# Kernel optimization log

Hardware: AMD Instinct MI355X
Metric: run time of the kernel (lower is better)

The kernel has to match this reference:

```python
import jax, jax.numpy as jnp
import numpy as np

B, T, E = 4, 2048, 1024
H = 16
HS = E // H  # head_size = d_model // num_heads, d_model == E here
D_FF = 4 * E
EPS = 1e-5


def _layernorm(x, g, b):
    mu = jnp.mean(x, axis=-1, keepdims=True)
    var = jnp.var(x, axis=-1, keepdims=True)
    return (x - mu) * jax.lax.rsqrt(var + EPS) * g + b


def setup_inputs() -> dict:
    key = jax.random.key(0)
    ks = jax.random.split(key, 12)
    s_e = 1.0 / np.sqrt(E)
    s_ff = 1.0 / np.sqrt(D_FF)
    return {
        "x": jax.random.normal(ks[0], (B, T, E), jnp.float32),
        "ln1_g": jnp.ones((E,), jnp.float32),
        "ln1_b": jnp.zeros((E,), jnp.float32),
        "Wq": jax.random.normal(ks[1], (E, E), jnp.float32) * s_e,
        "bq": jnp.zeros((E,), jnp.float32),
        "Wk": jax.random.normal(ks[2], (E, E), jnp.float32) * s_e,
        "bk": jnp.zeros((E,), jnp.float32),
        "Wv": jax.random.normal(ks[3], (E, E), jnp.float32) * s_e,
        "bv": jnp.zeros((E,), jnp.float32),
        "Wp": jax.random.normal(ks[4], (E, E), jnp.float32) * s_e,
        "bp": jnp.zeros((E,), jnp.float32),
        "ln2_g": jnp.ones((E,), jnp.float32),
        "ln2_b": jnp.zeros((E,), jnp.float32),
        "W1": jax.random.normal(ks[5], (E, D_FF), jnp.float32) * s_e,
        "b1": jnp.zeros((D_FF,), jnp.float32),
        "W2": jax.random.normal(ks[6], (D_FF, E), jnp.float32) * s_ff,
        "b2": jnp.zeros((E,), jnp.float32),
    }


def reference(x, ln1_g, ln1_b, Wq, bq, Wk, bk, Wv, bv, Wp, bp,
              ln2_g, ln2_b, W1, b1, W2, b2):
    # --- attention sublayer ---
    h = _layernorm(x, ln1_g, ln1_b)                      # [B,T,E]
    q = (h @ Wq + bq).reshape(B, T, H, HS)
    k = (h @ Wk + bk).reshape(B, T, H, HS)
    v = (h @ Wv + bv).reshape(B, T, H, HS)
    scores = jnp.einsum('bqhd,bkhd->bhqk', q, k) * (HS ** -0.5)  # [B,H,T,T]
    causal = jnp.tril(jnp.ones((T, T), bool))
    scores = jnp.where(causal, scores, -jnp.inf)
    w = jax.nn.softmax(scores, axis=-1)
    attn = jnp.einsum('bhqk,bkhd->bqhd', w, v).reshape(B, T, H * HS)
    x = x + attn @ Wp + bp
    # --- FFN sublayer ---
    h2 = _layernorm(x, ln2_g, ln2_b)
    x = x + jax.nn.relu(h2 @ W1 + b1) @ W2 + b2
    return x
```

## Files before the change

### kernel.cpp

```cpp
#include <hip/hip_runtime.h>
#include <hip/hip_bf16.h>

#define B_ 4
#define T_ 2048
#define E_ 1024
#define H_ 16
#define HS_ 64
#define DFF_ 4096
#define M_ (B_ * T_)
#define LDQ_ (3 * E_)

typedef __bf16 bf16_t;
typedef __bf16 bf16x4 __attribute__((ext_vector_type(4)));
typedef __bf16 bf16x8 __attribute__((ext_vector_type(8)));
typedef float f32x4 __attribute__((ext_vector_type(4)));

#define AS1 __attribute__((address_space(1)))
#define AS3 __attribute__((address_space(3)))

__device__ __forceinline__ void gload_lds16(const void* g, void* l) {
  __builtin_amdgcn_global_load_lds((AS1 void*)(g), (AS3 void*)(l), 16, 0, 0);
}

__global__ __launch_bounds__(256) void wtrans_kernel(
    const float* __restrict__ W, bf16_t* __restrict__ Wt, int Krows, int Ncols) {
  __shared__ float tile[32][33];
  int tx = threadIdx.x, ty = threadIdx.y;
  int n0 = blockIdx.x * 32, k0 = blockIdx.y * 32;
#pragma unroll
  for (int i = 0; i < 32; i += 8)
    tile[ty + i][tx] = W[(long)(k0 + ty + i) * Ncols + n0 + tx];
  __syncthreads();
#pragma unroll
  for (int i = 0; i < 32; i += 8)
    Wt[(long)(n0 + ty + i) * Krows + k0 + tx] = (bf16_t)tile[tx][ty + i];
}

__global__ __launch_bounds__(256) void bcat_kernel(const float* a, const float* b,
                                                   const float* c, float* o) {
  int i = blockIdx.x * 256 + threadIdx.x;
  o[i] = i < 1024 ? a[i] : (i < 2048 ? b[i - 1024] : c[i - 2048]);
}

__global__ __launch_bounds__(256) void layernorm_kernel(
    const float* __restrict__ in, const float* __restrict__ g,
    const float* __restrict__ b, bf16_t* __restrict__ out) {
  int row = blockIdx.x;
  int tid = threadIdx.x;
  const float4* inr = (const float4*)(in + (long)row * E_);
  float4 v = inr[tid];
  float s = v.x + v.y + v.z + v.w;
  float ss = v.x * v.x + v.y * v.y + v.z * v.z + v.w * v.w;
#pragma unroll
  for (int o = 32; o; o >>= 1) {
    s += __shfl_xor(s, o);
    ss += __shfl_xor(ss, o);
  }
  __shared__ float red[8];
  int wv = tid >> 6;
  if ((tid & 63) == 0) {
    red[wv] = s;
    red[4 + wv] = ss;
  }
  __syncthreads();
  s = red[0] + red[1] + red[2] + red[3];
  ss = red[4] + red[5] + red[6] + red[7];
  float mu = s * (1.f / E_);
  float var = ss * (1.f / E_) - mu * mu;
  float rs = rsqrtf(var + 1e-5f);
  int ci = tid * 4;
  float4 gv = *(const float4*)(g + ci);
  float4 bv = *(const float4*)(b + ci);
  long o0 = (long)row * E_ + ci;
  out[o0 + 0] = (bf16_t)((v.x - mu) * rs * gv.x + bv.x);
  out[o0 + 1] = (bf16_t)((v.y - mu) * rs * gv.y + bv.y);
  out[o0 + 2] = (bf16_t)((v.z - mu) * rs * gv.z + bv.z);
  out[o0 + 3] = (bf16_t)((v.w - mu) * rs * gv.w + bv.w);
}

template <int RELU>
__global__ __launch_bounds__(512, 2) void gemm256_kernel(
    const bf16_t* __restrict__ A, const bf16_t* __restrict__ Bt,
    const float* __restrict__ bias, bf16_t* __restrict__ out, int N, int K) {
  __shared__ bf16_t As0[256 * 32], As1[256 * 32], As2[256 * 32], As3[256 * 32];
  __shared__ bf16_t Bs0[256 * 32], Bs1[256 * 32], Bs2[256 * 32], Bs3[256 * 32];
  const int tid = threadIdx.x;
  const int wave = tid >> 6;
  const int lane = tid & 63;
  const int wr = wave >> 2;
  const int wc = wave & 3;
  const int quad = lane >> 4, l16 = lane & 15;

  const int gx = gridDim.x;
  const int id = blockIdx.y * gx + blockIdx.x;
  const int xcd = id & 7;
  const int k_ = id >> 3;
  const int bxr = k_ % gx;
  const int byr = (k_ / gx) * 8 + xcd;
  const long rowBase = (long)byr * 256;
  const long colBase = (long)bxr * 256;

  f32x4 acc[8][4] = {};

  const int ntiles = K >> 5;

  auto stageA = [&](bf16_t* dst, int t) {
    const int k0 = t << 5;
#pragma unroll
    for (int p = 0; p < 2; ++p) {
      int idx = p * 512 + tid;
      int row = idx >> 2;
      int col = (idx & 3) * 8;
      gload_lds16(&A[(rowBase + row) * K + k0 + col],
                  dst + (p * 512 + wave * 64) * 8);
    }
  };
  auto stageB = [&](bf16_t* dst, int t) {
    const int k0 = t << 5;
#pragma unroll
    for (int p = 0; p < 2; ++p) {
      int idx = p * 512 + tid;
      int row = idx >> 2;
      int col = (idx & 3) * 8;
      gload_lds16(&Bt[(colBase + row) * K + k0 + col],
                  dst + (p * 512 + wave * 64) * 8);
    }
  };

  auto tileStep = [&](int t, const bf16_t* as, const bf16_t* bs, bf16_t* nA,
                      bf16_t* nB) {
    const bool pre = (t + 3 < ntiles);
    bf16x8 bfrag[4];
#pragma unroll
    for (int fc = 0; fc < 4; ++fc)
      bfrag[fc] = *(const bf16x8*)&bs[(wc * 64 + fc * 16 + l16) * 32 + quad * 8];

    {
      bf16x8 afrag[4];
#pragma unroll
      for (int fr = 0; fr < 4; ++fr)
        afrag[fr] =
            *(const bf16x8*)&as[(wr * 128 + fr * 16 + l16) * 32 + quad * 8];
      if (pre) stageA(nA, t + 3);
      __builtin_amdgcn_s_setprio(1);
#pragma unroll
      for (int fr = 0; fr < 4; ++fr)
#pragma unroll
        for (int fc = 0; fc < 4; ++fc)
          acc[fr][fc] = __builtin_amdgcn_mfma_f32_16x16x32_bf16(
              afrag[fr], bfrag[fc], acc[fr][fc], 0, 0, 0);
      __builtin_amdgcn_s_setprio(0);
      __builtin_amdgcn_s_barrier();
    }
    {
      bf16x8 afrag[4];
#pragma unroll
      for (int fr = 0; fr < 4; ++fr)
        afrag[fr] = *(const bf16x8*)&as[(wr * 128 + 64 + fr * 16 + l16) * 32 +
                                        quad * 8];
      if (pre) stageB(nB, t + 3);
      __builtin_amdgcn_s_setprio(1);
#pragma unroll
      for (int fr = 0; fr < 4; ++fr)
#pragma unroll
        for (int fc = 0; fc < 4; ++fc)
          acc[4 + fr][fc] = __builtin_amdgcn_mfma_f32_16x16x32_bf16(
              afrag[fr], bfrag[fc], acc[4 + fr][fc], 0, 0, 0);
      __builtin_amdgcn_s_setprio(0);
      if (t + 3 < ntiles)
        asm volatile("s_waitcnt vmcnt(8)" ::: "memory");
      else if (t + 2 < ntiles)
        asm volatile("s_waitcnt vmcnt(4)" ::: "memory");
      else if (t + 1 < ntiles)
        asm volatile("s_waitcnt vmcnt(0)" ::: "memory");
      if (t + 1 < ntiles) __builtin_amdgcn_s_barrier();
    }
  };

  stageA(As0, 0); stageB(Bs0, 0);
  stageA(As1, 1); stageB(Bs1, 1);
  stageA(As2, 2); stageB(Bs2, 2);
  asm volatile("s_waitcnt vmcnt(8)" ::: "memory");
  __builtin_amdgcn_s_barrier();

  for (int t = 0; t < ntiles; t += 4) {
    tileStep(t + 0, As0, Bs0, As3, Bs3);
    tileStep(t + 1, As1, Bs1, As0, Bs0);
    tileStep(t + 2, As2, Bs2, As1, Bs1);
    tileStep(t + 3, As3, Bs3, As2, Bs2);
  }

#pragma unroll
  for (int mh = 0; mh < 2; ++mh)
#pragma unroll
    for (int fr = 0; fr < 4; ++fr)
#pragma unroll
      for (int fc = 0; fc < 4; ++fc) {
        int colg = (int)colBase + wc * 64 + fc * 16 + l16;
        float bv = bias[colg];
#pragma unroll
        for (int r = 0; r < 4; ++r) {
          long rowg = rowBase + wr * 128 + mh * 64 + fr * 16 + quad * 4 + r;
          float v = acc[mh * 4 + fr][fc][r] + bv;
          if (RELU) v = fmaxf(v, 0.f);
          out[rowg * N + colg] = (bf16_t)v;
        }
      }
}

template <int MODE>
__global__ __launch_bounds__(512, 1) void gemm256x128_kernel(
    const bf16_t* __restrict__ A, const bf16_t* __restrict__ Bt,
    const float* __restrict__ bias, const float* __restrict__ resid,
    void* __restrict__ out, bf16_t* __restrict__ vt_out, int N, int K) {
  __shared__ bf16_t As0[256 * 32], As1[256 * 32], As2[256 * 32], As3[256 * 32];
  __shared__ bf16_t Bs0[128 * 32], Bs1[128 * 32], Bs2[128 * 32], Bs3[128 * 32];
  const int tid = threadIdx.x;
  const int wave = tid >> 6;
  const int lane = tid & 63;
  const int wr = wave >> 1;
  const int wc = wave & 1;
  const int quad = lane >> 4, l16 = lane & 15;

  const int gx = gridDim.x;
  const int id = blockIdx.y * gx + blockIdx.x;
  const int xcd = id & 7;
  const int k_ = id >> 3;
  const int bxr = k_ % gx;
  const int byr = (k_ / gx) * 8 + xcd;
  const long rowBase = (long)byr * 256;
  const long colBase = (long)bxr * 128;

  f32x4 acc[4][4] = {};

  const int ntiles = K >> 5;

  auto stageA = [&](bf16_t* dst, int t) {
    const int k0 = t << 5;
#pragma unroll
    for (int p = 0; p < 2; ++p) {
      int idx = p * 512 + tid;
      int row = idx >> 2;
      int col = (idx & 3) * 8;
      gload_lds16(&A[(rowBase + row) * K + k0 + col],
                  dst + (p * 512 + wave * 64) * 8);
    }
  };
  auto stageB = [&](bf16_t* dst, int t) {
    const int k0 = t << 5;
    int row = tid >> 2;
    int col = (tid & 3) * 8;
    gload_lds16(&Bt[(colBase + row) * K + k0 + col], dst + (wave * 64) * 8);
  };

  auto tileStep = [&](int t, const bf16_t* as, const bf16_t* bs, bf16_t* nA,
                      bf16_t* nB) {
    const bool pre = (t + 3 < ntiles);
    bf16x8 bfrag[4];
#pragma unroll
    for (int fc = 0; fc < 4; ++fc)
      bfrag[fc] = *(const bf16x8*)&bs[(wc * 64 + fc * 16 + l16) * 32 + quad * 8];

    {
      bf16x8 afrag[2];
#pragma unroll
      for (int fr = 0; fr < 2; ++fr)
        afrag[fr] =
            *(const bf16x8*)&as[(wr * 64 + fr * 16 + l16) * 32 + quad * 8];
      if (pre) stageA(nA, t + 3);
      __builtin_amdgcn_s_setprio(1);
#pragma unroll
      for (int fr = 0; fr < 2; ++fr)
#pragma unroll
        for (int fc = 0; fc < 4; ++fc)
          acc[fr][fc] = __builtin_amdgcn_mfma_f32_16x16x32_bf16(
              afrag[fr], bfrag[fc], acc[fr][fc], 0, 0, 0);
      __builtin_amdgcn_s_setprio(0);
      __builtin_amdgcn_s_barrier();
    }
    {
      bf16x8 afrag[2];
#pragma unroll
      for (int fr = 2; fr < 4; ++fr)
        afrag[fr - 2] =
            *(const bf16x8*)&as[(wr * 64 + fr * 16 + l16) * 32 + quad * 8];
      if (pre) stageB(nB, t + 3);
      __builtin_amdgcn_s_setprio(1);
#pragma unroll
      for (int fr = 2; fr < 4; ++fr)
#pragma unroll
        for (int fc = 0; fc < 4; ++fc)
          acc[fr][fc] = __builtin_amdgcn_mfma_f32_16x16x32_bf16(
              afrag[fr - 2], bfrag[fc], acc[fr][fc], 0, 0, 0);
      __builtin_amdgcn_s_setprio(0);
      if (t + 3 < ntiles)
        asm volatile("s_waitcnt vmcnt(6)" ::: "memory");
      else if (t + 2 < ntiles)
        asm volatile("s_waitcnt vmcnt(3)" ::: "memory");
      else if (t + 1 < ntiles)
        asm volatile("s_waitcnt vmcnt(0)" ::: "memory");
      if (t + 1 < ntiles) __builtin_amdgcn_s_barrier();
    }
  };

  stageA(As0, 0); stageB(Bs0, 0);
  stageA(As1, 1); stageB(Bs1, 1);
  stageA(As2, 2); stageB(Bs2, 2);
  asm volatile("s_waitcnt vmcnt(6)" ::: "memory");
  __builtin_amdgcn_s_barrier();

  for (int t = 0; t < ntiles; t += 4) {
    tileStep(t + 0, As0, Bs0, As3, Bs3);
    tileStep(t + 1, As1, Bs1, As0, Bs0);
    tileStep(t + 2, As2, Bs2, As1, Bs1);
    tileStep(t + 3, As3, Bs3, As2, Bs2);
  }

#pragma unroll
  for (int fr = 0; fr < 4; ++fr)
#pragma unroll
    for (int fc = 0; fc < 4; ++fc) {
      int colg = (int)colBase + wc * 64 + fc * 16 + l16;
      float bv = bias[colg];
#pragma unroll
      for (int r = 0; r < 4; ++r) {
        long rowg = rowBase + wr * 64 + fr * 16 + quad * 4 + r;
        float v = acc[fr][fc][r] + bv;
        long idx = rowg * N + colg;
        if (MODE == 1) {
          ((float*)out)[idx] = v + resid[idx];
        } else {
          ((bf16_t*)out)[idx] = (bf16_t)v;
          if (MODE == 2 && colg >= 2 * E_) {
            int d = colg & 63;
            int hh2 = (colg - 2 * E_) >> 6;
            int bb = (int)(rowg >> 11);
            int tt = (int)(rowg & 2047);
            vt_out[(((long)(bb * 16 + hh2)) * 64 + d) * T_ + tt] = (bf16_t)v;
          }
        }
      }
    }
}

__global__ __launch_bounds__(512) void flash_attn_kernel(
    const bf16_t* __restrict__ qkv, const bf16_t* __restrict__ vt,
    bf16_t* __restrict__ attn, bf16_t* __restrict__ Opart,
    float* __restrict__ mlpart) {
  int gx = 14 - (int)blockIdx.x;
  int pt = 0, sp = 0;
  for (int p = 0; p < 8; ++p) {
    int ns = (2 * p + 1) / 6 + 1;
    if (gx < ns) { pt = p; sp = gx; break; }
    gx -= ns;
  }

  const int tid = threadIdx.x;
  const int wave = tid >> 6;
  const int half = wave >> 2;
  const int wsub = wave & 3;
  const int lane = tid & 63;
  const int quad = lane >> 4, l16 = lane & 15;
  const int bh = blockIdx.y, b = bh >> 4, hh = bh & 15;

  const int ti = 2 * pt + half;
  const int nsplit = ti / 6 + 1;
  const int qw = ti * 128 + wsub * 32;
  const int jbeg = 12 * sp;
  const int jendU = min(12 * sp + 12, 4 * pt + 4);

  __shared__ __align__(16) bf16_t Ks[2][64 * 64];
  __shared__ __align__(16) bf16_t Vs[2][64 * 64];
  __shared__ __align__(16) bf16_t Ps[8][16 * 64];

  const bf16_t* qb = qkv;
  const bf16_t* kb = qkv + E_;

  bf16x8 aq[2][2];
#pragma unroll
  for (int s = 0; s < 2; ++s) {
    long base = (long)(b * T_ + qw + s * 16 + l16) * LDQ_ + hh * HS_ + quad * 8;
    aq[s][0] = *(const bf16x8*)&qb[base];
    aq[s][1] = *(const bf16x8*)&qb[base + 32];
#pragma unroll
    for (int e = 0; e < 8; ++e) {
      aq[s][0][e] = (bf16_t)((float)aq[s][0][e] * 0.125f);
      aq[s][1][e] = (bf16_t)((float)aq[s][1][e] * 0.125f);
    }
  }

  f32x4 o[2][4] = {};
  float lsum[2] = {};

  auto stage = [&](int buf, int j) {
    const int kv0 = j * 64;
    int row = tid >> 3;
    int gcol = ((tid & 7) ^ (row & 7)) * 8;
    gload_lds16(&kb[(long)(b * T_ + kv0 + row) * LDQ_ + hh * HS_ + gcol],
                &Ks[buf][wave * 512]);
    gload_lds16(&vt[((long)bh * HS_ + row) * T_ + kv0 + gcol],
                &Vs[buf][wave * 512]);
  };

  stage(0, jbeg);
  __syncthreads();

  for (int j = jbeg; j < jendU; ++j) {
    const int kv0 = j * 64;
    const int cur = (j - jbeg) & 1;
    if (j + 1 < jendU) stage(cur ^ 1, j + 1);
    const bf16_t* KsL = Ks[cur];
    const bf16_t* VsL = Vs[cur];
    bf16_t* Pw = Ps[wave];

#pragma unroll
    for (int s = 0; s < 2; ++s) {
      const int qs = qw + s * 16;
      if (kv0 <= qs + 15) {
        f32x4 sc[4];
        __builtin_amdgcn_s_setprio(1);
#pragma unroll
        for (int sub = 0; sub < 4; ++sub) {
          const int rk = sub * 16 + l16;
          const int k0 = rk * 64 + ((quad ^ (rk & 7)) * 8);
          f32x4 t = {};
          t = __builtin_amdgcn_mfma_f32_16x16x32_bf16(
              *(const bf16x8*)&KsL[k0], aq[s][0], t, 0, 0, 0);
          t = __builtin_amdgcn_mfma_f32_16x16x32_bf16(
              *(const bf16x8*)&KsL[k0 ^ 32], aq[s][1], t, 0, 0, 0);
          sc[sub] = t;
        }
        __builtin_amdgcn_s_setprio(0);
        if (kv0 + 63 > qs) {
          int qcol = qs + l16;
#pragma unroll
          for (int sub = 0; sub < 4; ++sub)
#pragma unroll
            for (int r = 0; r < 4; ++r) {
              int kvrow = kv0 + sub * 16 + quad * 4 + r;
              if (kvrow > qcol) sc[sub][r] = -INFINITY;
            }
        }
        float part = 0.f;
#pragma unroll
        for (int sub = 0; sub < 4; ++sub) {
#pragma unroll
          for (int r = 0; r < 4; ++r) sc[sub][r] = __expf(sc[sub][r]);
          part += (sc[sub][0] + sc[sub][1]) + (sc[sub][2] + sc[sub][3]);
        }
        lsum[s] += part;
#pragma unroll
        for (int sub = 0; sub < 4; ++sub) {
          bf16x4 pk;
#pragma unroll
          for (int r = 0; r < 4; ++r) pk[r] = (bf16_t)sc[sub][r];
          const int ch = sub * 2 + (quad >> 1);
          const int off = ((ch ^ (l16 & 7)) * 8) + ((quad & 1) * 4);
          *(bf16x4*)&Pw[l16 * 64 + off] = pk;
        }
        const int p0 = l16 * 64 + ((quad ^ (l16 & 7)) * 8);
        bf16x8 ap0 = *(const bf16x8*)&Pw[p0];
        bf16x8 ap1 = *(const bf16x8*)&Pw[p0 ^ 32];
        __builtin_amdgcn_s_setprio(1);
#pragma unroll
        for (int nt = 0; nt < 4; ++nt) {
          const int rv = nt * 16 + l16;
          const int v0 = rv * 64 + ((quad ^ (rv & 7)) * 8);
          o[s][nt] = __builtin_amdgcn_mfma_f32_16x16x32_bf16(
              *(const bf16x8*)&VsL[v0], ap0, o[s][nt], 0, 0, 0);
          o[s][nt] = __builtin_amdgcn_mfma_f32_16x16x32_bf16(
              *(const bf16x8*)&VsL[v0 ^ 32], ap1, o[s][nt], 0, 0, 0);
        }
        __builtin_amdgcn_s_setprio(0);
      }
    }
    __syncthreads();
  }

  float lval[2];
#pragma unroll
  for (int s = 0; s < 2; ++s) {
    float v = lsum[s];
    v += __shfl_xor(v, 16);
    v += __shfl_xor(v, 32);
    lval[s] = v;
  }

  if (nsplit == 1) {
#pragma unroll
    for (int s = 0; s < 2; ++s) {
      float inv = 1.f / lval[s];
      long rowg = (long)b * T_ + qw + s * 16 + l16;
#pragma unroll
      for (int nt = 0; nt < 4; ++nt) {
        bf16x4 pk;
#pragma unroll
        for (int r = 0; r < 4; ++r) pk[r] = (bf16_t)(o[s][nt][r] * inv);
        *(bf16x4*)&attn[rowg * E_ + hh * HS_ + nt * 16 + quad * 4] = pk;
      }
    }
  } else {
    int idx = (ti < 12) ? (ti - 6) * 2 + sp : 12 + (ti - 12) * 3 + sp;
    long slot = (long)bh * 24 + idx;
    bf16_t* op = Opart + slot * (128 * 64);
    float* ml = mlpart + slot * 256;
#pragma unroll
    for (int s = 0; s < 2; ++s) {
      float inv = 1.f / lval[s];
      int rloc = wsub * 32 + s * 16 + l16;
#pragma unroll
      for (int nt = 0; nt < 4; ++nt) {
        bf16x4 pk;
#pragma unroll
        for (int r = 0; r < 4; ++r) pk[r] = (bf16_t)(o[s][nt][r] * inv);
        *(bf16x4*)&op[rloc * 64 + nt * 16 + quad * 4] = pk;
      }
      if (quad == 0) ml[rloc] = lval[s];
    }
  }
}

__global__ __launch_bounds__(256) void flash_merge_kernel(
    const bf16_t* __restrict__ Opart, const float* __restrict__ mlpart,
    bf16_t* __restrict__ attn) {
  int ti = 6 + blockIdx.x;
  int bh = blockIdx.y, b = bh >> 4, hh = bh & 15;
  int ns = ti / 6 + 1;
  int base_idx = (ti < 12) ? (ti - 6) * 2 : 12 + (ti - 12) * 3;
  int r = threadIdx.x >> 1;
  int dh = (threadIdx.x & 1) * 32;

  float w[3], den = 0.f;
  for (int s = 0; s < ns; ++s) {
    long slot = (long)bh * 24 + base_idx + s;
    w[s] = mlpart[slot * 256 + r];
    den += w[s];
  }
  float inv = 1.f / den;
  float acc[32];
#pragma unroll
  for (int d = 0; d < 32; ++d) acc[d] = 0.f;
  for (int s = 0; s < ns; ++s) {
    long slot = (long)bh * 24 + base_idx + s;
    const bf16_t* op = Opart + slot * (128 * 64) + r * 64 + dh;
#pragma unroll
    for (int d = 0; d < 32; ++d) acc[d] += w[s] * (float)op[d];
  }
  long rowg = (long)b * T_ + ti * 128 + r;
  bf16_t* dst = attn + rowg * E_ + hh * HS_ + dh;
#pragma unroll
  for (int d = 0; d < 32; ++d) dst[d] = (bf16_t)(acc[d] * inv);
}

extern "C" void kernel_launch(void* const* d_in, const int* in_sizes, int n_in,
                              void* d_out, int out_size, void* d_ws,
                              size_t ws_size, hipStream_t stream) {
  const float* x = (const float*)d_in[0];
  const float* ln1_g = (const float*)d_in[1];
  const float* ln1_b = (const float*)d_in[2];
  const float* Wq = (const float*)d_in[3];
  const float* bq = (const float*)d_in[4];
  const float* Wk = (const float*)d_in[5];
  const float* bk = (const float*)d_in[6];
  const float* Wv = (const float*)d_in[7];
  const float* bv = (const float*)d_in[8];
  const float* Wp = (const float*)d_in[9];
  const float* bp = (const float*)d_in[10];
  const float* ln2_g = (const float*)d_in[11];
  const float* ln2_b = (const float*)d_in[12];
  const float* W1 = (const float*)d_in[13];
  const float* b1 = (const float*)d_in[14];
  const float* W2 = (const float*)d_in[15];
  const float* b2 = (const float*)d_in[16];
  float* out = (float*)d_out;

  const size_t MB = 1ull << 20;
  char* ws = (char*)d_ws;
  bf16_t* wqkvt = (bf16_t*)(ws + 0 * MB);
  bf16_t* wpt   = (bf16_t*)(ws + 6 * MB);
  bf16_t* w1t   = (bf16_t*)(ws + 8 * MB);
  bf16_t* w2t   = (bf16_t*)(ws + 16 * MB);
  float*  bqkv  = (float*)(ws + 24 * MB);
  bf16_t* h     = (bf16_t*)(ws + 25 * MB);
  bf16_t* qkvb  = (bf16_t*)(ws + 41 * MB);
  bf16_t* vt    = (bf16_t*)(ws + 89 * MB);
  float*  xmid  = (float*)(ws + 105 * MB);
  bf16_t* Opart = (bf16_t*)(ws + 105 * MB);
  float* mlpart = (float*)(ws + 131 * MB);
  bf16_t* attn  = h;
  bf16_t* h2    = h;
  bf16_t* ff1   = qkvb;

  dim3 tb(32, 8);
  wtrans_kernel<<<dim3(E_ / 32, E_ / 32), tb, 0, stream>>>(Wq, wqkvt, E_, E_);
  wtrans_kernel<<<dim3(E_ / 32, E_ / 32), tb, 0, stream>>>(Wk, wqkvt + (long)E_ * E_, E_, E_);
  wtrans_kernel<<<dim3(E_ / 32, E_ / 32), tb, 0, stream>>>(Wv, wqkvt + 2l * E_ * E_, E_, E_);
  wtrans_kernel<<<dim3(E_ / 32, E_ / 32), tb, 0, stream>>>(Wp, wpt, E_, E_);
  wtrans_kernel<<<dim3(DFF_ / 32, E_ / 32), tb, 0, stream>>>(W1, w1t, E_, DFF_);
  wtrans_kernel<<<dim3(E_ / 32, DFF_ / 32), tb, 0, stream>>>(W2, w2t, DFF_, E_);
  bcat_kernel<<<12, 256, 0, stream>>>(bq, bk, bv, bqkv);

  layernorm_kernel<<<M_, 256, 0, stream>>>(x, ln1_g, ln1_b, h);

  gemm256x128_kernel<2><<<dim3(3 * E_ / 128, M_ / 256), 512, 0, stream>>>(
      h, wqkvt, bqkv, nullptr, qkvb, vt, 3 * E_, E_);

  flash_attn_kernel<<<dim3(15, B_ * H_), 512, 0, stream>>>(qkvb, vt, attn,
                                                           Opart, mlpart);
  flash_merge_kernel<<<dim3(10, B_ * H_), 256, 0, stream>>>(Opart, mlpart, attn);

  gemm256x128_kernel<1><<<dim3(E_ / 128, M_ / 256), 512, 0, stream>>>(
      attn, wpt, bp, x, xmid, nullptr, E_, E_);

  layernorm_kernel<<<M_, 256, 0, stream>>>(xmid, ln2_g, ln2_b, h2);

  gemm256_kernel<1><<<dim3(DFF_ / 256, M_ / 256), 512, 0, stream>>>(
      h2, w1t, b1, ff1, DFF_, E_);
  gemm256x128_kernel<1><<<dim3(E_ / 128, M_ / 256), 512, 0, stream>>>(
      ff1, w2t, b2, xmid, out, nullptr, E_, DFF_);
}
```

Baseline: 512.3 us.

## Cut GEMM LDS to triple buffering for two blocks per CU; split V transpose

```diff
diff --git a/kernel.cpp b/kernel.cpp
--- a/kernel.cpp
+++ b/kernel.cpp
@@ -209,12 +209,12 @@
 }
 
 template <int MODE>
-__global__ __launch_bounds__(512, 1) void gemm256x128_kernel(
+__global__ __launch_bounds__(512, 2) void gemm256x128_kernel(
     const bf16_t* __restrict__ A, const bf16_t* __restrict__ Bt,
     const float* __restrict__ bias, const float* __restrict__ resid,
-    void* __restrict__ out, bf16_t* __restrict__ vt_out, int N, int K) {
-  __shared__ bf16_t As0[256 * 32], As1[256 * 32], As2[256 * 32], As3[256 * 32];
-  __shared__ bf16_t Bs0[128 * 32], Bs1[128 * 32], Bs2[128 * 32], Bs3[128 * 32];
+    void* __restrict__ out, int N, int K) {
+  __shared__ bf16_t As0[256 * 32], As1[256 * 32], As2[256 * 32];
+  __shared__ bf16_t Bs0[128 * 32], Bs1[128 * 32], Bs2[128 * 32];
   const int tid = threadIdx.x;
   const int wave = tid >> 6;
   const int lane = tid & 63;
@@ -255,7 +255,7 @@
 
   auto tileStep = [&](int t, const bf16_t* as, const bf16_t* bs, bf16_t* nA,
                       bf16_t* nB) {
-    const bool pre = (t + 3 < ntiles);
+    const bool pre = (t + 2 < ntiles);
     bf16x8 bfrag[4];
 #pragma unroll
     for (int fc = 0; fc < 4; ++fc)
@@ -267,7 +267,7 @@
       for (int fr = 0; fr < 2; ++fr)
         afrag[fr] =
             *(const bf16x8*)&as[(wr * 64 + fr * 16 + l16) * 32 + quad * 8];
-      if (pre) stageA(nA, t + 3);
+      if (pre) stageA(nA, t + 2);
       __builtin_amdgcn_s_setprio(1);
 #pragma unroll
       for (int fr = 0; fr < 2; ++fr)
@@ -284,7 +284,7 @@
       for (int fr = 2; fr < 4; ++fr)
         afrag[fr - 2] =
             *(const bf16x8*)&as[(wr * 64 + fr * 16 + l16) * 32 + quad * 8];
-      if (pre) stageB(nB, t + 3);
+      if (pre) stageB(nB, t + 2);
       __builtin_amdgcn_s_setprio(1);
 #pragma unroll
       for (int fr = 2; fr < 4; ++fr)
@@ -293,9 +293,7 @@
           acc[fr][fc] = __builtin_amdgcn_mfma_f32_16x16x32_bf16(
               afrag[fr - 2], bfrag[fc], acc[fr][fc], 0, 0, 0);
       __builtin_amdgcn_s_setprio(0);
-      if (t + 3 < ntiles)
-        asm volatile("s_waitcnt vmcnt(6)" ::: "memory");
-      else if (t + 2 < ntiles)
+      if (t + 2 < ntiles)
         asm volatile("s_waitcnt vmcnt(3)" ::: "memory");
       else if (t + 1 < ntiles)
         asm volatile("s_waitcnt vmcnt(0)" ::: "memory");
@@ -305,15 +303,14 @@
 
   stageA(As0, 0); stageB(Bs0, 0);
   stageA(As1, 1); stageB(Bs1, 1);
-  stageA(As2, 2); stageB(Bs2, 2);
-  asm volatile("s_waitcnt vmcnt(6)" ::: "memory");
+  asm volatile("s_waitcnt vmcnt(3)" ::: "memory");
   __builtin_amdgcn_s_barrier();
 
-  for (int t = 0; t < ntiles; t += 4) {
-    tileStep(t + 0, As0, Bs0, As3, Bs3);
-    tileStep(t + 1, As1, Bs1, As0, Bs0);
-    tileStep(t + 2, As2, Bs2, As1, Bs1);
-    tileStep(t + 3, As3, Bs3, As2, Bs2);
+  int t = 0;
+  while (true) {
+    tileStep(t, As0, Bs0, As2, Bs2); if (++t >= ntiles) break;
+    tileStep(t, As1, Bs1, As0, Bs0); if (++t >= ntiles) break;
+    tileStep(t, As2, Bs2, As1, Bs1); if (++t >= ntiles) break;
   }
 
 #pragma unroll
@@ -327,20 +324,31 @@
         long rowg = rowBase + wr * 64 + fr * 16 + quad * 4 + r;
         float v = acc[fr][fc][r] + bv;
         long idx = rowg * N + colg;
-        if (MODE == 1) {
+        if (MODE == 0) {
+          ((bf16_t*)out)[idx] = (bf16_t)v;
+        } else {
           ((float*)out)[idx] = v + resid[idx];
-        } else {
-          ((bf16_t*)out)[idx] = (bf16_t)v;
-          if (MODE == 2 && colg >= 2 * E_) {
-            int d = colg & 63;
-            int hh2 = (colg - 2 * E_) >> 6;
-            int bb = (int)(rowg >> 11);
-            int tt = (int)(rowg & 2047);
-            vt_out[(((long)(bb * 16 + hh2)) * 64 + d) * T_ + tt] = (bf16_t)v;
-          }
         }
       }
     }
+}
+
+__global__ __launch_bounds__(256) void vtrans_kernel(
+    const bf16_t* __restrict__ qkv, bf16_t* __restrict__ vt) {
+  __shared__ bf16_t tile[32][33];
+  int tx = threadIdx.x, ty = threadIdx.y;
+  int t0 = blockIdx.x * 32;
+  int d0 = (blockIdx.y & 1) * 32;
+  int bh = blockIdx.y >> 1;
+  int b = bh >> 4, hh = bh & 15;
+#pragma unroll
+  for (int i = 0; i < 32; i += 8)
+    tile[ty + i][tx] =
+        qkv[(long)(b * T_ + t0 + ty + i) * LDQ_ + 2 * E_ + hh * HS_ + d0 + tx];
+  __syncthreads();
+#pragma unroll
+  for (int i = 0; i < 32; i += 8)
+    vt[((long)bh * HS_ + d0 + ty + i) * T_ + t0 + tx] = tile[tx][ty + i];
 }
 
 __global__ __launch_bounds__(512) void flash_attn_kernel(
@@ -602,20 +610,22 @@
 
   layernorm_kernel<<<M_, 256, 0, stream>>>(x, ln1_g, ln1_b, h);
 
-  gemm256x128_kernel<2><<<dim3(3 * E_ / 128, M_ / 256), 512, 0, stream>>>(
-      h, wqkvt, bqkv, nullptr, qkvb, vt, 3 * E_, E_);
+  gemm256x128_kernel<0><<<dim3(3 * E_ / 128, M_ / 256), 512, 0, stream>>>(
+      h, wqkvt, bqkv, nullptr, qkvb, 3 * E_, E_);
+
+  vtrans_kernel<<<dim3(T_ / 32, 2 * B_ * H_), tb, 0, stream>>>(qkvb, vt);
 
   flash_attn_kernel<<<dim3(15, B_ * H_), 512, 0, stream>>>(qkvb, vt, attn,
                                                            Opart, mlpart);
   flash_merge_kernel<<<dim3(10, B_ * H_), 256, 0, stream>>>(Opart, mlpart, attn);
 
   gemm256x128_kernel<1><<<dim3(E_ / 128, M_ / 256), 512, 0, stream>>>(
-      attn, wpt, bp, x, xmid, nullptr, E_, E_);
+      attn, wpt, bp, x, xmid, E_, E_);
 
   layernorm_kernel<<<M_, 256, 0, stream>>>(xmid, ln2_g, ln2_b, h2);
 
   gemm256_kernel<1><<<dim3(DFF_ / 256, M_ / 256), 512, 0, stream>>>(
       h2, w1t, b1, ff1, DFF_, E_);
   gemm256x128_kernel<1><<<dim3(E_ / 128, M_ / 256), 512, 0, stream>>>(
-      ff1, w2t, b2, xmid, out, nullptr, E_, DFF_);
-}
+      ff1, w2t, b2, xmid, out, E_, DFF_);
+}
```

New measurement: 492.1 us. 1.04x faster.
